# Kernel optimization log

Hardware: AMD Instinct MI355X
Metric: run time of the kernel (lower is better)

## Reference

```python
import jax, jax.numpy as jnp
import numpy as np

H_FWD, H_REV, M = 25, 25, 3        # n=3, m=3 hardcoded in module
IN_SIZE = 4 * H_REV + 1            # 101 = H_rev + (n-2) + H_rev*m
UNITS = 512
BATCH = 8192
INPUT_SIZE = H_REV + (3 - 2) + (H_FWD + H_REV) * M  # 176


def setup_inputs() -> dict:
    key = jax.random.key(0)
    ks = jax.random.split(key, 6)
    x = jax.random.normal(ks[0], (BATCH, INPUT_SIZE), jnp.float32)

    def lin(k, fi, fo):
        kw, kb = jax.random.split(k)
        W = jax.random.normal(kw, (fi, fo), jnp.float32) / np.float32(np.sqrt(fi))
        b = jax.random.normal(kb, (fo,), jnp.float32) * 0.01
        return W, b

    W0, b0 = lin(ks[1], IN_SIZE, UNITS)
    W1, b1 = lin(ks[2], UNITS, UNITS)
    W2, b2 = lin(ks[3], UNITS, UNITS)
    W3, b3 = lin(ks[4], UNITS, UNITS)
    W4, b4 = lin(ks[5], UNITS, 1)
    return dict(x=x, W0=W0, b0=b0, W1=W1, b1=b1, W2=W2, b2=b2,
                W3=W3, b3=b3, W4=W4, b4=b4)


def _mlp(params, d):
    # Tanh MLP, final Linear to scalar; returns (B,)
    h = d
    for W, b in params[:-1]:
        h = jnp.tanh(h @ W + b)
    W, b = params[-1]
    return (h @ W + b)[:, 0]


def reference(x, W0, b0, W1, b1, W2, b2, W3, b3, W4, b4):
    params = [(W0, b0), (W1, b1), (W2, b2), (W3, b3), (W4, b4)]
    B = x.shape[0]
    e = x[:, :H_REV]                                   # (B, H_rev)
    v = x[:, -(H_FWD + H_REV) * M:].reshape(B, H_FWD + H_REV, M)
    f = lambda d: _mlp(params, d)

    w_cols, grads = [], []
    for i in range(H_FWD):  # strictly sequential recursion over horizon
        if i < H_REV:
            if i > 0:
                w_seg = jax.lax.stop_gradient(jnp.stack(w_cols, axis=1))
            else:
                w_seg = jnp.zeros((B, 0), x.dtype)
            data = jnp.concatenate(
                [e[:, i:], w_seg,
                 v[:, i:i + H_REV].reshape(B, -1),
                 jnp.full((B, 1), float(i), x.dtype)], axis=1)
        else:
            w_seg = jax.lax.stop_gradient(jnp.stack(w_cols[i - H_REV:i], axis=1))
            data = jnp.concatenate(
                [w_seg, v[:, i:i + H_REV].reshape(B, -1),
                 jnp.full((B, 1), float(i), x.dtype)], axis=1)
        out, vjp_fn = jax.vjp(f, data)      # out: (B,), scalar output per sample
        g, = vjp_fn(jnp.ones_like(out))     # (B, IN_SIZE): per-step Jacobian row
        w_cols.append(out)
        grads.append(g)

    w = jnp.stack(w_cols, axis=1)           # (B, H_fwd)
    grad = jnp.stack(grads, axis=1)         # (B, H_fwd, IN_SIZE)
    return w, grad
```

## Files before the change

kernel.cpp:

```cpp
#include <hip/hip_runtime.h>

#define B_ROWS 8192
#define UNITS 512
#define NITER 25
#define INSZ 176
#define KPAD 128
#define GRAD_COLS 101

typedef __attribute__((ext_vector_type(8))) short short8;
typedef __attribute__((ext_vector_type(4))) float f32x4;
typedef __attribute__((ext_vector_type(8))) _Float16 half8;

__device__ __forceinline__ unsigned short f2h_bits(float f) {
  _Float16 h = (_Float16)f;
  return __builtin_bit_cast(unsigned short, h);
}
__device__ __forceinline__ float h2f_bits(unsigned short b) {
  return (float)__builtin_bit_cast(_Float16, b);
}
__device__ __forceinline__ float fast_tanh(float x) {
  float e = __expf(2.0f * x);
  return 1.0f - 2.0f / (e + 1.0f);
}

typedef __attribute__((address_space(3))) unsigned int lds_u32;
typedef __attribute__((address_space(1))) const unsigned int glb_u32;
__device__ __forceinline__ void gload16(const void* g, void* l) {
  __builtin_amdgcn_global_load_lds((glb_u32*)g, (lds_u32*)l, 16, 0, 0);
}

struct GArgs {
  const unsigned short *A;
  const unsigned short *B;
  int K;
  const float* bias;
  const unsigned short *Hh;
  unsigned short *Oh;
  float* Og;
  int iter;
};

__global__ __launch_bounds__(256)
void prep_kernel(const float* __restrict__ W0, const float* __restrict__ W1,
                 const float* __restrict__ W2, const float* __restrict__ W3,
                 unsigned short* TW0, unsigned short* TW1,
                 unsigned short* TW2, unsigned short* TW3,
                 unsigned short* CW0, unsigned short* CW1,
                 unsigned short* CW2, unsigned short* CW3)
{
  int id = blockIdx.x * 256 + threadIdx.x;
  if (id < 512 * KPAD) {
    int n = id >> 7, k = id & (KPAD - 1);
    TW0[id] = f2h_bits((k < 101) ? W0[(size_t)k * 512 + n] : 0.0f);
    int n2 = id >> 9, k2 = id & 511;
    CW0[id] = f2h_bits((n2 < 101) ? W0[(size_t)n2 * 512 + k2] : 0.0f);
  }
  {
    int n = id >> 9, k = id & 511;
    TW1[id] = f2h_bits(W1[(size_t)k * 512 + n]);
    TW2[id] = f2h_bits(W2[(size_t)k * 512 + n]);
    TW3[id] = f2h_bits(W3[(size_t)k * 512 + n]);
    CW1[id] = f2h_bits(W1[id]);
    CW2[id] = f2h_bits(W2[id]);
    CW3[id] = f2h_bits(W3[id]);
  }
}

__global__ __launch_bounds__(256)
void build_d_kernel(const float* __restrict__ x, unsigned short* __restrict__ D)
{
  int id = blockIdx.x * 256 + threadIdx.x;
  int b = id >> 7, c = id & 127;
  float val;
  if (c < 25)             val = x[(size_t)b * INSZ + c];
  else if (c < 100)       val = x[(size_t)b * INSZ + 26 + (c - 25)];
  else                    val = 0.0f;
  D[id] = f2h_bits(val);
}

template<int EPI>
__device__ __forceinline__ void gemm_body(const GArgs g, short* smem, int id)
{
  const int t = threadIdx.x;
  const int w = t >> 6;
  const int lane = t & 63;
  const int l15 = lane & 15, l4 = lane >> 4;
  const int bm = (EPI == 2) ? id : (id & 63);
  const int bn = (EPI == 2) ? 0  : (id >> 6);
  const int wm = (w >> 1) * 64, wn = (w & 1) * 64;
  const int K = g.K;
  const int NK = K >> 6;
  f32x4 acc[4][4] = {};

  const int sr = t >> 3;
  const int ss = t & 7;

  auto stage = [&](int ks, int buf) {
    short* As = smem + buf * 16384;
    short* Bs = As + 8192;
    int kc = ks << 6;
#pragma unroll
    for (int q = 0; q < 4; ++q) {
      int r = q * 32 + sr;
      int c = ss ^ (r & 7);
      size_t ga = (size_t)(bm * 128 + r) * K + kc + c * 8;
      size_t gb = (size_t)(bn * 128 + r) * K + kc + c * 8;
      int ldst = q * 2048 + w * 512;
      gload16(g.A + ga, &As[ldst]);
      gload16(g.B + gb, &Bs[ldst]);
    }
  };

  stage(0, 0);
  __syncthreads();

  for (int ks = 0; ks < NK; ++ks) {
    if (ks + 1 < NK) stage(ks + 1, (ks + 1) & 1);
    const short* As = smem + (ks & 1) * 16384;
    const short* Bs = As + 8192;
#pragma unroll
    for (int kk = 0; kk < 2; ++kk) {
      short8 av[4], bh[4];
#pragma unroll
      for (int mi = 0; mi < 4; ++mi) {
        int row = wm + mi * 16 + l15;
        int eoff = row * 64 + (((kk * 4 + l4) ^ (row & 7)) << 3);
        av[mi] = *(const short8*)&As[eoff];
      }
#pragma unroll
      for (int ni = 0; ni < 4; ++ni) {
        int row = wn + ni * 16 + l15;
        int eoff = row * 64 + (((kk * 4 + l4) ^ (row & 7)) << 3);
        bh[ni] = *(const short8*)&Bs[eoff];
      }
#pragma unroll
      for (int mi = 0; mi < 4; ++mi)
#pragma unroll
        for (int ni = 0; ni < 4; ++ni)
          acc[mi][ni] = __builtin_amdgcn_mfma_f32_16x16x32_f16(
              __builtin_bit_cast(half8, av[mi]), __builtin_bit_cast(half8, bh[ni]),
              acc[mi][ni], 0, 0, 0);
    }
    __syncthreads();
  }

  const int gm0 = bm * 128 + wm;
  const int gn0 = bn * 128 + wn;
#pragma unroll
  for (int mi = 0; mi < 4; ++mi) {
#pragma unroll
    for (int ni = 0; ni < 4; ++ni) {
      int n = gn0 + ni * 16 + l15;
#pragma unroll
      for (int r = 0; r < 4; ++r) {
        int m = gm0 + mi * 16 + l4 * 4 + r;
        float v = acc[mi][ni][r];
        if constexpr (EPI == 0) {
          float h = fast_tanh(v + g.bias[n]);
          g.Oh[(size_t)m * UNITS + n] = f2h_bits(h);
        } else if constexpr (EPI == 1) {
          size_t idx = (size_t)m * UNITS + n;
          float h = h2f_bits(g.Hh[idx]);
          g.Oh[idx] = f2h_bits(v * (1.0f - h * h));
        } else {
          if (n < GRAD_COLS)
            g.Og[((size_t)m * NITER + g.iter) * GRAD_COLS + n] = v;
        }
      }
    }
  }
}

template<int EA, int EB>
__global__ __launch_bounds__(256, 2)
void paired_kernel(GArgs A, GArgs B, int nA) {
  __shared__ short smem[32768];
  int id = blockIdx.x;
  if (id < nA) gemm_body<EA>(A, smem, id);
  else         gemm_body<EB>(B, smem, id - nA);
}

template<int E>
__global__ __launch_bounds__(256, 2)
void solo_kernel(GArgs A) {
  __shared__ short smem[32768];
  gemm_body<E>(A, smem, blockIdx.x);
}

__global__ __launch_bounds__(256)
void dot_bd_kernel(const unsigned short* __restrict__ H3,
                   const float* __restrict__ W4, const float* __restrict__ b4,
                   const float* __restrict__ x, float* __restrict__ w_out,
                   unsigned short* __restrict__ U,
                   unsigned short* __restrict__ D,
                   int iter, int buildD)
{
  int w = threadIdx.x >> 6, lane = threadIdx.x & 63;
  int b = blockIdx.x * 4 + w;
  size_t base = (size_t)b * UNITS + lane * 8;
  short8 vh = *(const short8*)&H3[base];
  float dot = 0.0f;
  short8 ou;
#pragma unroll
  for (int j = 0; j < 8; ++j) {
    float h = h2f_bits((unsigned short)vh[j]);
    float g = W4[lane * 8 + j];
    dot += h * g;
    ou[j] = (short)f2h_bits((1.0f - h * h) * g);
  }
  *(short8*)&U[base] = ou;
#pragma unroll
  for (int off = 1; off < 64; off <<= 1) dot += __shfl_xor(dot, off);
  float wv = dot + b4[0];
  if (lane == 0) w_out[(size_t)b * NITER + iter] = wv;

  if (buildD) {
    int jn = iter + 1;
#pragma unroll
    for (int cc = 0; cc < 2; ++cc) {
      int c = lane + cc * 64;
      float val;
      if (c < 25 - jn)        val = x[(size_t)b * INSZ + jn + c];
      else if (c < 24)        val = w_out[(size_t)b * NITER + (c - (25 - jn))];
      else if (c == 24)       val = wv;
      else if (c < 100)       val = x[(size_t)b * INSZ + 26 + 3 * jn + (c - 25)];
      else if (c == 100)      val = (float)jn;
      else                    val = 0.0f;
      D[(size_t)b * KPAD + c] = f2h_bits(val);
    }
  }
}

extern "C" void kernel_launch(void* const* d_in, const int* in_sizes, int n_in,
                              void* d_out, int out_size, void* d_ws, size_t ws_size,
                              hipStream_t stream) {
  const float* x  = (const float*)d_in[0];
  const float* W0 = (const float*)d_in[1];
  const float* b0 = (const float*)d_in[2];
  const float* W1 = (const float*)d_in[3];
  const float* b1 = (const float*)d_in[4];
  const float* W2 = (const float*)d_in[5];
  const float* b2 = (const float*)d_in[6];
  const float* W3 = (const float*)d_in[7];
  const float* b3 = (const float*)d_in[8];
  const float* W4 = (const float*)d_in[9];
  const float* b4 = (const float*)d_in[10];

  float* w_out    = (float*)d_out;
  float* grad_out = (float*)d_out + (size_t)B_ROWS * NITER;

  char* p = (char*)d_ws;
  auto alloc = [&](size_t elems) { unsigned short* r = (unsigned short*)p; p += elems * 2; return r; };

  unsigned short* TW0 = alloc(512 * KPAD);
  unsigned short* TW1 = alloc(512 * 512);
  unsigned short* TW2 = alloc(512 * 512);
  unsigned short* TW3 = alloc(512 * 512);
  unsigned short* CW0 = alloc(KPAD * 512);
  unsigned short* CW1 = alloc(512 * 512);
  unsigned short* CW2 = alloc(512 * 512);
  unsigned short* CW3 = alloc(512 * 512);

  unsigned short* D = alloc((size_t)B_ROWS * KPAD);

  unsigned short *H[2][4];
  for (int par = 0; par < 2; ++par)
    for (int l = 0; l < 4; ++l)
      H[par][l] = alloc((size_t)B_ROWS * UNITS);
  unsigned short* Ua = alloc((size_t)B_ROWS * UNITS);
  unsigned short* Ub = alloc((size_t)B_ROWS * UNITS);

  prep_kernel<<<1024, 256, 0, stream>>>(W0, W1, W2, W3,
      TW0, TW1, TW2, TW3, CW0, CW1, CW2, CW3);

  build_d_kernel<<<4096, 256, 0, stream>>>(x, D);

  {
    GArgs f0 = {D, TW0, KPAD, b0, nullptr, H[0][0], nullptr, 0};
    GArgs f1 = {H[0][0], TW1, 512, b1, nullptr, H[0][1], nullptr, 0};
    GArgs f2 = {H[0][1], TW2, 512, b2, nullptr, H[0][2], nullptr, 0};
    GArgs f3 = {H[0][2], TW3, 512, b3, nullptr, H[0][3], nullptr, 0};
    solo_kernel<0><<<256, 256, 0, stream>>>(f0);
    solo_kernel<0><<<256, 256, 0, stream>>>(f1);
    solo_kernel<0><<<256, 256, 0, stream>>>(f2);
    solo_kernel<0><<<256, 256, 0, stream>>>(f3);
  }

  for (int i = 0; i < NITER; ++i) {
    int pp = i & 1, q = pp ^ 1;
    bool more = (i < NITER - 1);

    dot_bd_kernel<<<2048, 256, 0, stream>>>(H[pp][3], W4, b4, x, w_out,
                                            Ua, D, i, more ? 1 : 0);

    GArgs bw3 = {Ua, CW3, 512, nullptr, H[pp][2], Ub, nullptr, 0};
    GArgs bw2 = {Ub, CW2, 512, nullptr, H[pp][1], Ua, nullptr, 0};
    GArgs bw1 = {Ua, CW1, 512, nullptr, H[pp][0], Ub, nullptr, 0};
    GArgs gr0 = {Ub, CW0, 512, nullptr, nullptr, nullptr, grad_out, i};

    if (more) {
      GArgs f0 = {D, TW0, KPAD, b0, nullptr, H[q][0], nullptr, 0};
      GArgs f1 = {H[q][0], TW1, 512, b1, nullptr, H[q][1], nullptr, 0};
      GArgs f2 = {H[q][1], TW2, 512, b2, nullptr, H[q][2], nullptr, 0};
      GArgs f3 = {H[q][2], TW3, 512, b3, nullptr, H[q][3], nullptr, 0};
      paired_kernel<1, 0><<<512, 256, 0, stream>>>(bw3, f0, 256);
      paired_kernel<1, 0><<<512, 256, 0, stream>>>(bw2, f1, 256);
      paired_kernel<1, 0><<<512, 256, 0, stream>>>(bw1, f2, 256);
      paired_kernel<2, 0><<<320, 256, 0, stream>>>(gr0, f3, 64);
    } else {
      solo_kernel<1><<<256, 256, 0, stream>>>(bw3);
      solo_kernel<1><<<256, 256, 0, stream>>>(bw2);
      solo_kernel<1><<<256, 256, 0, stream>>>(bw1);
      solo_kernel<2><<<64, 256, 0, stream>>>(gr0);
    }
  }

  (void)in_sizes; (void)n_in; (void)out_size; (void)ws_size;
}
```

Measured before the change: 2.002 ms.

## Replace LDS-staged GEMM with direct global-to-register fragment loads

Drops the shared-memory double-buffered staging, where global_load_lds copies swizzled tiles into LDS. Each wave now loads its MFMA fragments straight from global memory into registers, keeping four k-steps in flight as a software pipeline. Block-to-tile mapping is also remapped so groups of 8 M-tiles share N-tiles, for better L2 reuse. This removes LDS traffic and most barriers, but raises VGPR pressure and loses the sharing of loaded tiles between waves. Global reads become strided and uncoalesced, and the same data is reread by multiple waves.

```diff
diff --git a/kernel.cpp b/kernel.cpp
--- a/kernel.cpp
+++ b/kernel.cpp
@@ -21,12 +21,6 @@
 __device__ __forceinline__ float fast_tanh(float x) {
   float e = __expf(2.0f * x);
   return 1.0f - 2.0f / (e + 1.0f);
-}
-
-typedef __attribute__((address_space(3))) unsigned int lds_u32;
-typedef __attribute__((address_space(1))) const unsigned int glb_u32;
-__device__ __forceinline__ void gload16(const void* g, void* l) {
-  __builtin_amdgcn_global_load_lds((glb_u32*)g, (lds_u32*)l, 16, 0, 0);
 }
 
 struct GArgs {
@@ -78,70 +72,59 @@
   D[id] = f2h_bits(val);
 }
 
+struct Frag { short8 a[4], b[4]; };
+
+__device__ __forceinline__ Frag loadf(const unsigned short* Ab, const unsigned short* Bb,
+                                      int K, int ks) {
+  Frag f;
+#pragma unroll
+  for (int i = 0; i < 4; ++i) {
+    f.a[i] = *(const short8*)(Ab + (size_t)i * 16 * K + ks * 32);
+    f.b[i] = *(const short8*)(Bb + (size_t)i * 16 * K + ks * 32);
+  }
+  return f;
+}
+
+__device__ __forceinline__ void mfma_step(const Frag& f, f32x4 (&acc)[4][4]) {
+#pragma unroll
+  for (int mi = 0; mi < 4; ++mi)
+#pragma unroll
+    for (int ni = 0; ni < 4; ++ni)
+      acc[mi][ni] = __builtin_amdgcn_mfma_f32_16x16x32_f16(
+          __builtin_bit_cast(half8, f.a[mi]), __builtin_bit_cast(half8, f.b[ni]),
+          acc[mi][ni], 0, 0, 0);
+}
+
 template<int EPI>
-__device__ __forceinline__ void gemm_body(const GArgs g, short* smem, int id)
+__device__ __forceinline__ void gemm_body(const GArgs g, int id)
 {
   const int t = threadIdx.x;
   const int w = t >> 6;
   const int lane = t & 63;
   const int l15 = lane & 15, l4 = lane >> 4;
-  const int bm = (EPI == 2) ? id : (id & 63);
-  const int bn = (EPI == 2) ? 0  : (id >> 6);
+  const int bm = (EPI == 2) ? id : ((id & 7) | ((id >> 5) << 3));
+  const int bn = (EPI == 2) ? 0  : ((id >> 3) & 3);
   const int wm = (w >> 1) * 64, wn = (w & 1) * 64;
   const int K = g.K;
-  const int NK = K >> 6;
+  const int NK = K >> 5;
   f32x4 acc[4][4] = {};
 
-  const int sr = t >> 3;
-  const int ss = t & 7;
-
-  auto stage = [&](int ks, int buf) {
-    short* As = smem + buf * 16384;
-    short* Bs = As + 8192;
-    int kc = ks << 6;
-#pragma unroll
-    for (int q = 0; q < 4; ++q) {
-      int r = q * 32 + sr;
-      int c = ss ^ (r & 7);
-      size_t ga = (size_t)(bm * 128 + r) * K + kc + c * 8;
-      size_t gb = (size_t)(bn * 128 + r) * K + kc + c * 8;
-      int ldst = q * 2048 + w * 512;
-      gload16(g.A + ga, &As[ldst]);
-      gload16(g.B + gb, &Bs[ldst]);
-    }
-  };
-
-  stage(0, 0);
-  __syncthreads();
-
-  for (int ks = 0; ks < NK; ++ks) {
-    if (ks + 1 < NK) stage(ks + 1, (ks + 1) & 1);
-    const short* As = smem + (ks & 1) * 16384;
-    const short* Bs = As + 8192;
-#pragma unroll
-    for (int kk = 0; kk < 2; ++kk) {
-      short8 av[4], bh[4];
-#pragma unroll
-      for (int mi = 0; mi < 4; ++mi) {
-        int row = wm + mi * 16 + l15;
-        int eoff = row * 64 + (((kk * 4 + l4) ^ (row & 7)) << 3);
-        av[mi] = *(const short8*)&As[eoff];
-      }
-#pragma unroll
-      for (int ni = 0; ni < 4; ++ni) {
-        int row = wn + ni * 16 + l15;
-        int eoff = row * 64 + (((kk * 4 + l4) ^ (row & 7)) << 3);
-        bh[ni] = *(const short8*)&Bs[eoff];
-      }
-#pragma unroll
-      for (int mi = 0; mi < 4; ++mi)
-#pragma unroll
-        for (int ni = 0; ni < 4; ++ni)
-          acc[mi][ni] = __builtin_amdgcn_mfma_f32_16x16x32_f16(
-              __builtin_bit_cast(half8, av[mi]), __builtin_bit_cast(half8, bh[ni]),
-              acc[mi][ni], 0, 0, 0);
-    }
-    __syncthreads();
+  const unsigned short* Ab = g.A + ((size_t)(bm * 128 + wm + l15) * K + l4 * 8);
+  const unsigned short* Bb = g.B + ((size_t)(bn * 128 + wn + l15) * K + l4 * 8);
+
+  Frag F0 = loadf(Ab, Bb, K, 0);
+  Frag F1 = loadf(Ab, Bb, K, 1);
+  Frag F2 = loadf(Ab, Bb, K, 2);
+  Frag F3 = loadf(Ab, Bb, K, 3);
+
+  const int NJ = NK >> 2;
+  for (int j = 0; j < NJ; ++j) {
+    int nb = j * 4 + 4;
+    mfma_step(F0, acc); if (nb + 0 < NK) F0 = loadf(Ab, Bb, K, nb + 0);
+    mfma_step(F1, acc); if (nb + 1 < NK) F1 = loadf(Ab, Bb, K, nb + 1);
+    mfma_step(F2, acc); if (nb + 2 < NK) F2 = loadf(Ab, Bb, K, nb + 2);
+    mfma_step(F3, acc); if (nb + 3 < NK) F3 = loadf(Ab, Bb, K, nb + 3);
+    __builtin_amdgcn_s_barrier();
   }
 
   const int gm0 = bm * 128 + wm;
@@ -174,17 +157,15 @@
 template<int EA, int EB>
 __global__ __launch_bounds__(256, 2)
 void paired_kernel(GArgs A, GArgs B, int nA) {
-  __shared__ short smem[32768];
   int id = blockIdx.x;
-  if (id < nA) gemm_body<EA>(A, smem, id);
-  else         gemm_body<EB>(B, smem, id - nA);
+  if (id < nA) gemm_body<EA>(A, id);
+  else         gemm_body<EB>(B, id - nA);
 }
 
 template<int E>
 __global__ __launch_bounds__(256, 2)
 void solo_kernel(GArgs A) {
-  __shared__ short smem[32768];
-  gemm_body<E>(A, smem, blockIdx.x);
+  gemm_body<E>(A, blockIdx.x);
 }
 
 __global__ __launch_bounds__(256)
```

After: 3.833 ms. +91.5%, slower.
